# Optimization experiments

Measured on AMD Instinct MI355X. Metric: run time of the kernel, lower is better.

Reference implementation:

```python
import jax, jax.numpy as jnp
import numpy as np

K, B, C, T, D, H = 4, 1024, 128, 64, 64, 4  # timeframes, batch, in-feat, seq(=embed!), embed, heads
HD = D // H
EPS = 1e-5


def setup_inputs() -> dict:
    key = jax.random.key(0)
    ks = jax.random.split(key, 8)
    s = lambda k, shape: jax.random.normal(k, shape, dtype=jnp.float32) * 0.05
    return {
        "feats": jax.random.normal(ks[0], (K, B, C, T), dtype=jnp.float32),
        "proj_w": s(ks[1], (K, D, C)),
        "proj_b": jnp.zeros((K, D), jnp.float32),
        "wq": s(ks[2], (K, D, D)),
        "wk": s(ks[3], (K, D, D)),
        "wv": s(ks[4], (K, D, D)),
        "bq": jnp.zeros((K, D), jnp.float32),
        "bk": jnp.zeros((K, D), jnp.float32),
        "bv": jnp.zeros((K, D), jnp.float32),
        "wo": s(ks[5], (K, D, D)),
        "bo": jnp.zeros((K, D), jnp.float32),
        "ng": jnp.ones((K, D), jnp.float32),
        "nb": jnp.zeros((K, D), jnp.float32),
        "tfw": jnp.full((K,), 1.0 / K, jnp.float32),
        "fg": jnp.ones((K * D,), jnp.float32),
        "fb": jnp.zeros((K * D,), jnp.float32),
    }


def _ln(x, g, b):
    m = x.mean(-1, keepdims=True)
    v = ((x - m) ** 2).mean(-1, keepdims=True)
    return (x - m) * jax.lax.rsqrt(v + EPS) * g + b


def reference(feats, proj_w, proj_b, wq, wk, wv, bq, bk, bv, wo, bo, ng, nb, tfw, fg, fb):
    # per-timeframe Linear on channel axis: [K,B,C,T] -> [K,B,D,T]
    proj = jnp.einsum('kbct,kdc->kbdt', feats, proj_w) + proj_b[:, None, :, None]
    ctx4 = jnp.transpose(proj, (1, 0, 2, 3))              # [B,K,D,T] (torch.stack dim=1)
    ctx = ctx4.reshape(B * D, K, T)                       # replicates torch .view(B*T,K,D); needs T==D
    N = B * D
    scale = 1.0 / np.sqrt(HD)
    outs = []
    for i in range(K):  # small fixed loop over K=4 distinct attention blocks
        q_in = ctx[:, i]                                  # [N,D] query = i-th row
        q = (q_in @ wq[i].T + bq[i]).reshape(N, H, HD)
        k = (ctx @ wk[i].T + bk[i]).reshape(N, K, H, HD)
        v = (ctx @ wv[i].T + bv[i]).reshape(N, K, H, HD)
        sc = jnp.einsum('nhe,nkhe->nhk', q, k) * scale    # [N,H,K]
        a = jax.nn.softmax(sc, axis=-1)
        o = jnp.einsum('nhk,nkhe->nhe', a, v).reshape(N, D)
        o = o @ wo[i].T + bo[i]
        outs.append(_ln(o + q_in, ng[i], nb[i]))          # residual + per-tf LayerNorm
    w = jax.nn.softmax(tfw)
    comb = jnp.stack(outs, axis=1) * w[None, :, None]     # [N,K,D] weighted fusion
    fused = comb.reshape(B, D, K * D)                     # torch .view(B,T,K*D)
    return _ln(fused, fg, fb)
```

## Files before the change

kernel.cpp:

```cpp
#include <hip/hip_runtime.h>
#include <math.h>

#define EPSV 1e-5f

typedef __attribute__((ext_vector_type(8))) short short8;
typedef __attribute__((ext_vector_type(4))) float float4v;

__device__ __forceinline__ unsigned short f2bf(float f) {
  unsigned int x = __float_as_uint(f);
  return (unsigned short)((x + 0x7fffu + ((x >> 16) & 1u)) >> 16);
}
__device__ __forceinline__ float bf2f(unsigned short u) {
  return __uint_as_float(((unsigned int)u) << 16);
}
__device__ __forceinline__ float wave_sum64(float v) {
  v += __shfl_xor(v, 1);
  v += __shfl_xor(v, 2);
  v += __shfl_xor(v, 4);
  v += __shfl_xor(v, 8);
  v += __shfl_xor(v, 16);
  v += __shfl_xor(v, 32);
  return v;
}
__device__ __forceinline__ float group16_sum(float v) {
  v += __shfl_xor(v, 1);
  v += __shfl_xor(v, 2);
  v += __shfl_xor(v, 4);
  v += __shfl_xor(v, 8);
  return v;
}
__device__ __forceinline__ void lds_fence() {
  asm volatile("s_waitcnt lgkmcnt(0)" ::: "memory");
}

__global__ __launch_bounds__(256) void prep_kernel(
    const float* __restrict__ pw, const float* __restrict__ wq,
    const float* __restrict__ wk, const float* __restrict__ wv,
    const float* __restrict__ wo, unsigned short* __restrict__ wph,
    unsigned short* __restrict__ wpl, unsigned short* __restrict__ wb) {
  int idx = blockIdx.x * 256 + threadIdx.x;
  if (idx < 32768) {
    float f = pw[idx];
    unsigned short h = f2bf(f);
    wph[idx] = h;
    wpl[idx] = f2bf(f - bf2f(h));
  } else {
    int e = idx - 32768;
    int mat = e >> 14, i = (e >> 12) & 3, r = e & 4095;
    const float* src = (mat == 0) ? wq : (mat == 1) ? wk : (mat == 2) ? wv : wo;
    wb[((i * 4 + mat) << 12) + r] = f2bf(src[(i << 12) + r]);
  }
}

__global__ __launch_bounds__(256, 4) void proj_kernel(
    const float* __restrict__ feats, const unsigned short* __restrict__ wph,
    const unsigned short* __restrict__ wpl, const float* __restrict__ pb,
    unsigned short* __restrict__ ctxbf) {
  int kb = blockIdx.x;
  int k = kb >> 10;
  int b = kb & 1023;

  __shared__ __align__(16) unsigned short FH[64 * 136];
  __shared__ __align__(16) unsigned short FL[64 * 136];

  int tid = threadIdx.x;
  const float* fsrc = feats + (size_t)kb * 8192;
  for (int u = tid; u < 2048; u += 256) {
    float4 f = *(const float4*)&fsrc[u * 4];
    int c = u >> 4;
    int t0 = (u & 15) * 4;
#pragma unroll
    for (int q = 0; q < 4; ++q) {
      float fv = (q == 0) ? f.x : (q == 1) ? f.y : (q == 2) ? f.z : f.w;
      unsigned short h = f2bf(fv);
      FH[(t0 + q) * 136 + c] = h;
      FL[(t0 + q) * 136 + c] = f2bf(fv - bf2f(h));
    }
  }
  __syncthreads();

  int w = tid >> 6, l = tid & 63;
  int l15 = l & 15, lq = l >> 4;

  const float4v zf = {0.0f, 0.0f, 0.0f, 0.0f};
  float4v acc[4] = {zf, zf, zf, zf};

  const unsigned short* whp = wph + k * 8192 + (w * 16 + l15) * 128 + lq * 8;
  const unsigned short* wlp = wpl + k * 8192 + (w * 16 + l15) * 128 + lq * 8;

#pragma unroll
  for (int kc = 0; kc < 4; ++kc) {
    short8 ah = *(const short8*)&whp[kc * 32];
    short8 al = *(const short8*)&wlp[kc * 32];
#pragma unroll
    for (int nt = 0; nt < 4; ++nt) {
      short8 bh = *(const short8*)&FH[(nt * 16 + l15) * 136 + kc * 32 + lq * 8];
      short8 bl = *(const short8*)&FL[(nt * 16 + l15) * 136 + kc * 32 + lq * 8];
      acc[nt] = __builtin_amdgcn_mfma_f32_16x16x32_bf16(ah, bh, acc[nt], 0, 0, 0);
      acc[nt] = __builtin_amdgcn_mfma_f32_16x16x32_bf16(ah, bl, acc[nt], 0, 0, 0);
      acc[nt] = __builtin_amdgcn_mfma_f32_16x16x32_bf16(al, bh, acc[nt], 0, 0, 0);
    }
  }

  float pbv[4];
#pragma unroll
  for (int r = 0; r < 4; ++r) pbv[r] = pb[k * 64 + w * 16 + lq * 4 + r];

  size_t base = ((size_t)b * 64 + k * 16 + w * 4 + lq) * 256;
#pragma unroll
  for (int nt = 0; nt < 4; ++nt)
#pragma unroll
    for (int r = 0; r < 4; ++r)
      ctxbf[base + r * 64 + nt * 16 + l15] = f2bf(acc[nt][r] + pbv[r]);
}

__global__ __launch_bounds__(256, 2) void attn_fused(
    const unsigned short* __restrict__ ctxbf,
    const unsigned short* __restrict__ wb,
    const float* __restrict__ bq, const float* __restrict__ bk,
    const float* __restrict__ bv, const float* __restrict__ bo,
    const float* __restrict__ ng, const float* __restrict__ nb,
    const float* __restrict__ tfw, float* __restrict__ out) {
  __shared__ __align__(16) unsigned short CTP[64 * 264];
  __shared__ __align__(16) unsigned short OSP[4][16 * 72];

  int tid = threadIdx.x;
  int w = tid >> 6, l = tid & 63;
  int l15 = l & 15, lq = l >> 4;

  {
    const unsigned short* csrc = ctxbf + ((size_t)blockIdx.x * 64 + w * 16) * 256;
#pragma unroll
    for (int u = 0; u < 8; ++u) {
      int e = u * 64 + l;
      int row = e >> 5, c8 = (e & 31) * 8;
      *(short8*)&CTP[(w * 16 + row) * 264 + c8] =
          *(const short8*)&csrc[row * 256 + c8];
    }
  }
  lds_fence();

  float tf0 = tfw[0], tf1 = tfw[1], tf2 = tfw[2], tf3 = tfw[3];
  float tm = fmaxf(fmaxf(tf0, tf1), fmaxf(tf2, tf3));
  float te0 = __expf(tf0 - tm), te1 = __expf(tf1 - tm);
  float te2 = __expf(tf2 - tm), te3 = __expf(tf3 - tm);
  float tden = te0 + te1 + te2 + te3;

  const unsigned short* arow = &CTP[(w * 16 + l15) * 264];
  const float4v zf = {0.0f, 0.0f, 0.0f, 0.0f};

#pragma unroll 1
  for (int i = 0; i < 4; ++i) {
#define WFRAG(m, nt, s)                                                        \
  (*(const short8*)&wb[((i * 4 + (m)) << 12) + ((nt)*16 + l15) * 64 +          \
                       (s)*32 + lq * 8])

    float wi = ((i == 0) ? te0 : (i == 1) ? te1 : (i == 2) ? te2 : te3) / tden;

    float bqv[4], bkv[4], bvv[4];
#pragma unroll
    for (int nt = 0; nt < 4; ++nt) {
      int d = i * 64 + nt * 16 + l15;
      bqv[nt] = bq[d]; bkv[nt] = bk[d]; bvv[nt] = bv[d];
    }

    float4v qacc[4] = {zf, zf, zf, zf};
#pragma unroll
    for (int s = 0; s < 2; ++s) {
      short8 af = *(const short8*)&arow[i * 64 + s * 32 + lq * 8];
#pragma unroll
      for (int nt = 0; nt < 4; ++nt)
        qacc[nt] = __builtin_amdgcn_mfma_f32_16x16x32_bf16(af, WFRAG(0, nt, s),
                                                           qacc[nt], 0, 0, 0);
    }
#pragma unroll
    for (int nt = 0; nt < 4; ++nt)
#pragma unroll
      for (int r = 0; r < 4; ++r) qacc[nt][r] += bqv[nt];

    short8 kf[2][4], vf[2][4];
#pragma unroll
    for (int s = 0; s < 2; ++s)
#pragma unroll
      for (int nt = 0; nt < 4; ++nt) {
        kf[s][nt] = WFRAG(1, nt, s);
        vf[s][nt] = WFRAG(2, nt, s);
      }

    float4v oacc[4] = {zf, zf, zf, zf};
    float lsum[4][4] = {{0,0,0,0},{0,0,0,0},{0,0,0,0},{0,0,0,0}};

#pragma unroll 1
    for (int j = 0; j < 4; ++j) {
      float4v kacc[4] = {zf, zf, zf, zf};
      float4v vacc[4] = {zf, zf, zf, zf};
#pragma unroll
      for (int s = 0; s < 2; ++s) {
        short8 af = *(const short8*)&arow[j * 64 + s * 32 + lq * 8];
#pragma unroll
        for (int nt = 0; nt < 4; ++nt) {
          kacc[nt] = __builtin_amdgcn_mfma_f32_16x16x32_bf16(af, kf[s][nt],
                                                             kacc[nt], 0, 0, 0);
          vacc[nt] = __builtin_amdgcn_mfma_f32_16x16x32_bf16(af, vf[s][nt],
                                                             vacc[nt], 0, 0, 0);
        }
      }
#pragma unroll
      for (int nt = 0; nt < 4; ++nt)
#pragma unroll
        for (int r = 0; r < 4; ++r) {
          float p = qacc[nt][r] * (kacc[nt][r] + bkv[nt]);
          p = group16_sum(p) * 0.25f;
          float e = __expf(p);
          lsum[nt][r] += e;
          oacc[nt][r] += e * (vacc[nt][r] + bvv[nt]);
        }
    }

    lds_fence();
#pragma unroll
    for (int nt = 0; nt < 4; ++nt)
#pragma unroll
      for (int r = 0; r < 4; ++r)
        OSP[w][(lq * 4 + r) * 72 + nt * 16 + l15] = f2bf(oacc[nt][r] / lsum[nt][r]);
    lds_fence();

    float4v o2[4] = {zf, zf, zf, zf};
#pragma unroll
    for (int s = 0; s < 2; ++s) {
      short8 af = *(const short8*)&OSP[w][l15 * 72 + s * 32 + lq * 8];
#pragma unroll
      for (int nt = 0; nt < 4; ++nt)
        o2[nt] = __builtin_amdgcn_mfma_f32_16x16x32_bf16(af, WFRAG(3, nt, s),
                                                         o2[nt], 0, 0, 0);
    }

    float bov[4], ngv[4], nbv[4];
#pragma unroll
    for (int nt = 0; nt < 4; ++nt) {
      int d = i * 64 + nt * 16 + l15;
      bov[nt] = bo[d]; ngv[nt] = ng[d]; nbv[nt] = nb[d];
    }

    float rr[4][4];
#pragma unroll
    for (int nt = 0; nt < 4; ++nt)
#pragma unroll
      for (int r = 0; r < 4; ++r) {
        float qin = bf2f(CTP[(w * 16 + lq * 4 + r) * 264 + i * 64 + nt * 16 + l15]);
        rr[nt][r] = o2[nt][r] + bov[nt] + qin;
      }

#pragma unroll
    for (int r = 0; r < 4; ++r) {
      float sm = group16_sum(rr[0][r] + rr[1][r] + rr[2][r] + rr[3][r]) * (1.0f / 64.0f);
      float vs = 0.0f;
#pragma unroll
      for (int nt = 0; nt < 4; ++nt) { float dx = rr[nt][r] - sm; vs += dx * dx; }
      vs = group16_sum(vs) * (1.0f / 64.0f);
      float inv = rsqrtf(vs + EPSV);
      size_t row = (size_t)blockIdx.x * 64 + w * 16 + lq * 4 + r;
#pragma unroll
      for (int nt = 0; nt < 4; ++nt) {
        float val = wi * ((rr[nt][r] - sm) * inv * ngv[nt] + nbv[nt]);
        out[row * 256 + i * 64 + nt * 16 + l15] = val;
      }
    }
#undef WFRAG
  }
}

__global__ __launch_bounds__(256, 4) void final_ln_kernel(
    float* __restrict__ out, const float* __restrict__ fg,
    const float* __restrict__ fb) {
  int lane = threadIdx.x & 63;
  int wave = threadIdx.x >> 6;
  size_t n = (size_t)blockIdx.x * 4 + wave;

  float4 v = *(const float4*)&out[n * 256 + lane * 4];
  float mean = wave_sum64(v.x + v.y + v.z + v.w) * (1.0f / 256.0f);
  float dx = v.x - mean, dy = v.y - mean, dz = v.z - mean, dw = v.w - mean;
  float var = wave_sum64(dx * dx + dy * dy + dz * dz + dw * dw) * (1.0f / 256.0f);
  float inv = rsqrtf(var + EPSV);

  float4 g = *(const float4*)&fg[lane * 4];
  float4 bb = *(const float4*)&fb[lane * 4];
  float4 o;
  o.x = dx * inv * g.x + bb.x;
  o.y = dy * inv * g.y + bb.y;
  o.z = dz * inv * g.z + bb.z;
  o.w = dw * inv * g.w + bb.w;
  *(float4*)&out[n * 256 + lane * 4] = o;
}

extern "C" void kernel_launch(void* const* d_in, const int* in_sizes, int n_in,
                              void* d_out, int out_size, void* d_ws, size_t ws_size,
                              hipStream_t stream) {
  const float* feats  = (const float*)d_in[0];
  const float* proj_w = (const float*)d_in[1];
  const float* proj_b = (const float*)d_in[2];
  const float* wq  = (const float*)d_in[3];
  const float* wk  = (const float*)d_in[4];
  const float* wv  = (const float*)d_in[5];
  const float* bq  = (const float*)d_in[6];
  const float* bk  = (const float*)d_in[7];
  const float* bv  = (const float*)d_in[8];
  const float* wo  = (const float*)d_in[9];
  const float* bo  = (const float*)d_in[10];
  const float* ng  = (const float*)d_in[11];
  const float* nb  = (const float*)d_in[12];
  const float* tfw = (const float*)d_in[13];
  const float* fg  = (const float*)d_in[14];
  const float* fb  = (const float*)d_in[15];
  float* out = (float*)d_out;

  unsigned short* ctxbf = (unsigned short*)d_ws;
  unsigned short* wph = (unsigned short*)((char*)d_ws + ((size_t)32 << 20));
  unsigned short* wpl = wph + 32768;
  unsigned short* wb  = wpl + 32768;

  prep_kernel<<<384, 256, 0, stream>>>(proj_w, wq, wk, wv, wo, wph, wpl, wb);
  proj_kernel<<<4096, 256, 0, stream>>>(feats, wph, wpl, proj_b, ctxbf);
  attn_fused<<<1024, 256, 0, stream>>>(ctxbf, wb, bq, bk, bv, bo,
                                       ng, nb, tfw, out);
  final_ln_kernel<<<16384, 256, 0, stream>>>(out, fg, fb);
}
```

Measured before the change: 358.1 us.

## Swizzle projection LDS tiles, add MFMA priority hints, raise attention occupancy

The projection kernel's feature staging is rewritten: each thread gathers 8 channels for one time step and writes 16-byte vectors into an XOR-swizzled, unpadded LDS layout. This replaces the scalar transposed stores and padding and aims to cut bank conflicts and store instruction count. Both kernels also wrap their MFMA loops in s_setprio hints so waves issuing matrix work get scheduling priority. The attention kernel's launch bound minimum blocks per CU goes from 2 to 3, which may force register spilling.

```diff
diff --git a/kernel.cpp b/kernel.cpp
--- a/kernel.cpp
+++ b/kernel.cpp
@@ -60,22 +60,29 @@
   int k = kb >> 10;
   int b = kb & 1023;
 
-  __shared__ __align__(16) unsigned short FH[64 * 136];
-  __shared__ __align__(16) unsigned short FL[64 * 136];
+  __shared__ __align__(16) unsigned short FH[64 * 128];
+  __shared__ __align__(16) unsigned short FL[64 * 128];
 
   int tid = threadIdx.x;
   const float* fsrc = feats + (size_t)kb * 8192;
-  for (int u = tid; u < 2048; u += 256) {
-    float4 f = *(const float4*)&fsrc[u * 4];
-    int c = u >> 4;
-    int t0 = (u & 15) * 4;
-#pragma unroll
-    for (int q = 0; q < 4; ++q) {
-      float fv = (q == 0) ? f.x : (q == 1) ? f.y : (q == 2) ? f.z : f.w;
-      unsigned short h = f2bf(fv);
-      FH[(t0 + q) * 136 + c] = h;
-      FL[(t0 + q) * 136 + c] = f2bf(fv - bf2f(h));
-    }
+#pragma unroll
+  for (int it = 0; it < 4; ++it) {
+    int e = it * 256 + tid;
+    int t = e & 63;
+    int cg = e >> 6;
+    float fv[8];
+#pragma unroll
+    for (int q = 0; q < 8; ++q) fv[q] = fsrc[(cg * 8 + q) * 64 + t];
+    short8 hv, lv;
+#pragma unroll
+    for (int q = 0; q < 8; ++q) {
+      unsigned short h = f2bf(fv[q]);
+      hv[q] = (short)h;
+      lv[q] = (short)f2bf(fv[q] - bf2f(h));
+    }
+    int u = cg ^ (t & 15);
+    *(short8*)&FH[t * 128 + u * 8] = hv;
+    *(short8*)&FL[t * 128 + u * 8] = lv;
   }
   __syncthreads();
 
@@ -88,19 +95,22 @@
   const unsigned short* whp = wph + k * 8192 + (w * 16 + l15) * 128 + lq * 8;
   const unsigned short* wlp = wpl + k * 8192 + (w * 16 + l15) * 128 + lq * 8;
 
+  __builtin_amdgcn_s_setprio(1);
 #pragma unroll
   for (int kc = 0; kc < 4; ++kc) {
     short8 ah = *(const short8*)&whp[kc * 32];
     short8 al = *(const short8*)&wlp[kc * 32];
 #pragma unroll
     for (int nt = 0; nt < 4; ++nt) {
-      short8 bh = *(const short8*)&FH[(nt * 16 + l15) * 136 + kc * 32 + lq * 8];
-      short8 bl = *(const short8*)&FL[(nt * 16 + l15) * 136 + kc * 32 + lq * 8];
+      int boff = (nt * 16 + l15) * 128 + (((kc * 4 + lq) ^ l15) * 8);
+      short8 bh = *(const short8*)&FH[boff];
+      short8 bl = *(const short8*)&FL[boff];
       acc[nt] = __builtin_amdgcn_mfma_f32_16x16x32_bf16(ah, bh, acc[nt], 0, 0, 0);
       acc[nt] = __builtin_amdgcn_mfma_f32_16x16x32_bf16(ah, bl, acc[nt], 0, 0, 0);
       acc[nt] = __builtin_amdgcn_mfma_f32_16x16x32_bf16(al, bh, acc[nt], 0, 0, 0);
     }
   }
+  __builtin_amdgcn_s_setprio(0);
 
   float pbv[4];
 #pragma unroll
@@ -114,7 +124,7 @@
       ctxbf[base + r * 64 + nt * 16 + l15] = f2bf(acc[nt][r] + pbv[r]);
 }
 
-__global__ __launch_bounds__(256, 2) void attn_fused(
+__global__ __launch_bounds__(256, 3) void attn_fused(
     const unsigned short* __restrict__ ctxbf,
     const unsigned short* __restrict__ wb,
     const float* __restrict__ bq, const float* __restrict__ bk,
@@ -165,6 +175,7 @@
     }
 
     float4v qacc[4] = {zf, zf, zf, zf};
+    __builtin_amdgcn_s_setprio(1);
 #pragma unroll
     for (int s = 0; s < 2; ++s) {
       short8 af = *(const short8*)&arow[i * 64 + s * 32 + lq * 8];
@@ -173,6 +184,7 @@
         qacc[nt] = __builtin_amdgcn_mfma_f32_16x16x32_bf16(af, WFRAG(0, nt, s),
                                                            qacc[nt], 0, 0, 0);
     }
+    __builtin_amdgcn_s_setprio(0);
 #pragma unroll
     for (int nt = 0; nt < 4; ++nt)
 #pragma unroll
@@ -194,6 +206,7 @@
     for (int j = 0; j < 4; ++j) {
       float4v kacc[4] = {zf, zf, zf, zf};
       float4v vacc[4] = {zf, zf, zf, zf};
+      __builtin_amdgcn_s_setprio(1);
 #pragma unroll
       for (int s = 0; s < 2; ++s) {
         short8 af = *(const short8*)&arow[j * 64 + s * 32 + lq * 8];
@@ -205,6 +218,7 @@
                                                              vacc[nt], 0, 0, 0);
         }
       }
+      __builtin_amdgcn_s_setprio(0);
 #pragma unroll
       for (int nt = 0; nt < 4; ++nt)
 #pragma unroll
@@ -226,6 +240,7 @@
     lds_fence();
 
     float4v o2[4] = {zf, zf, zf, zf};
+    __builtin_amdgcn_s_setprio(1);
 #pragma unroll
     for (int s = 0; s < 2; ++s) {
       short8 af = *(const short8*)&OSP[w][l15 * 72 + s * 32 + lq * 8];
@@ -234,6 +249,7 @@
         o2[nt] = __builtin_amdgcn_mfma_f32_16x16x32_bf16(af, WFRAG(3, nt, s),
                                                          o2[nt], 0, 0, 0);
     }
+    __builtin_amdgcn_s_setprio(0);
 
     float bov[4], ngv[4], nbv[4];
 #pragma unroll
```

Result: slower. 431.8 us (+20.6%).
